# Kernel tuning notes

Hardware: AMD Instinct MI355X
Metric: run time of the kernel (lower is better)

Reference implementation:

```python
import jax, jax.numpy as jnp
import numpy as np

NUM_HEADS = 12
WIN = 7  # window_size[0] == window_size[1]


def setup_inputs() -> dict:
    key = jax.random.key(0)
    ks = jax.random.split(key, 8)
    B_, N, C = 2048, WIN * WIN, 384
    nW = 64
    return {
        "x": jax.random.normal(ks[0], (B_, N, C), dtype=jnp.float32),
        "mask": jax.random.normal(ks[1], (nW, N, N), dtype=jnp.float32),
        "qkv_w": jax.random.normal(ks[2], (3 * C, C), dtype=jnp.float32) * 0.02,
        "qkv_b": jax.random.normal(ks[3], (3 * C,), dtype=jnp.float32) * 0.02,
        "proj_w": jax.random.normal(ks[4], (C, C), dtype=jnp.float32) * 0.02,
        "proj_b": jax.random.normal(ks[5], (C,), dtype=jnp.float32) * 0.02,
        "rpb_table": jax.random.normal(ks[6], ((2 * WIN - 1) ** 2, NUM_HEADS), dtype=jnp.float32) * 0.02,
        "rel_index": jax.random.randint(ks[7], (N * N,), 0, (2 * WIN - 1) ** 2, dtype=jnp.int32),
    }


def reference(x, mask, qkv_w, qkv_b, proj_w, proj_b, rpb_table, rel_index):
    B_, N, C = x.shape
    H = NUM_HEADS
    d = C // H
    scale = d ** -0.5

    # QKV projection (quant wrappers act as identity in non-quant state)
    qkv = x @ qkv_w.T + qkv_b                      # [B_, N, 3C]
    qkv = qkv.reshape(B_, N, 3, H, d).transpose(2, 0, 3, 1, 4)  # [3, B_, H, N, d]
    q, k, v = qkv[0], qkv[1], qkv[2]

    attn = jnp.einsum("bhnd,bhmd->bhnm", q * scale, k)  # [B_, H, N, N]

    # relative position bias gather: [N*N] -> [N, N, H] -> [H, N, N]
    bias = rpb_table[rel_index].reshape(N, N, H).transpose(2, 0, 1)
    attn = attn + bias[None]

    # shifted-window mask add
    nW = mask.shape[0]
    attn = attn.reshape(B_ // nW, nW, H, N, N) + mask[None, :, None]
    attn = attn.reshape(B_, H, N, N)

    attn = jax.nn.softmax(attn, axis=-1)

    out = jnp.einsum("bhnm,bhmd->bhnd", attn, v)   # [B_, H, N, d]
    out = out.transpose(0, 2, 1, 3).reshape(B_, N, C)
    out = out @ proj_w.T + proj_b
    return out, attn
```

## Files before the change

### kernel.cpp

```cpp
#include <hip/hip_runtime.h>
#include <hip/hip_bf16.h>
#include <stdint.h>

#define H_ 12
#define D_ 32
#define N_ 49
#define C_ 384
#define B_TOT 2048
#define BH 24576
#define M_ROWS 100352
#define SCALE 0.17677669529663689f

typedef float f32x4 __attribute__((ext_vector_type(4)));
typedef __bf16 bf16x8 __attribute__((ext_vector_type(8)));
typedef unsigned short ushortx8 __attribute__((ext_vector_type(8)));

static __device__ __forceinline__ unsigned short f2bf(float f) {
  __bf16 b = (__bf16)f;
  return __builtin_bit_cast(unsigned short, b);
}

static __device__ __forceinline__ uint4 pack8(float4 a, float4 b) {
  ushortx8 v;
  v[0] = f2bf(a.x); v[1] = f2bf(a.y); v[2] = f2bf(a.z); v[3] = f2bf(a.w);
  v[4] = f2bf(b.x); v[5] = f2bf(b.y); v[6] = f2bf(b.z); v[7] = f2bf(b.w);
  return __builtin_bit_cast(uint4, v);
}

#define GL16(gp, lp)                                                        \
  __builtin_amdgcn_global_load_lds(                                         \
      (const __attribute__((address_space(1))) unsigned int*)(gp),          \
      (__attribute__((address_space(3))) unsigned int*)(lp), 16, 0, 0)

__global__ void prep(const float* __restrict__ x, const float* __restrict__ wq,
                     const float* __restrict__ wpw, const float* __restrict__ mask,
                     const float* __restrict__ rpb, const int* __restrict__ ridx,
                     unsigned short* __restrict__ x_bf,
                     unsigned short* __restrict__ wq_bf,
                     unsigned short* __restrict__ wp_bf,
                     float* __restrict__ comb) {
  const int blk = blockIdx.x, tid = threadIdx.x;
  if (blk < 2048) {
    for (int i = blk * 256 + tid; i < 4816896; i += 2048 * 256) {
      float4 a = ((const float4*)x)[2 * i];
      float4 b = ((const float4*)x)[2 * i + 1];
      *(uint4*)&x_bf[(size_t)i * 8] = pack8(a, b);
    }
  } else if (blk < 2264) {
    const int i = (blk - 2048) * 256 + tid;
    float4 a = ((const float4*)wq)[2 * i];
    float4 b = ((const float4*)wq)[2 * i + 1];
    *(uint4*)&wq_bf[(size_t)i * 8] = pack8(a, b);
  } else if (blk < 2336) {
    const int i = (blk - 2264) * 256 + tid;
    float4 a = ((const float4*)wpw)[2 * i];
    float4 b = ((const float4*)wpw)[2 * i + 1];
    *(uint4*)&wp_bf[(size_t)i * 8] = pack8(a, b);
  } else {
    const int wh = blk - 2336;
    const int w = wh / 12, h = wh - w * 12;
    float* cb = comb + (size_t)wh * 4096;
    const float* mw = mask + (size_t)w * N_ * N_;
    for (int e = tid; e < 4096; e += 256) {
      const int r = e >> 6, c = e & 63;
      float v;
      if (c >= N_) v = -1e30f;
      else if (r >= N_) v = 0.0f;
      else v = mw[r * N_ + c] + rpb[ridx[r * N_ + c] * H_ + h];
      cb[(r * 16 + (c & 15)) * 4 + (c >> 4)] = v;
    }
  }
}

__global__ __launch_bounds__(256, 4)
void qkv_gemm(const unsigned short* __restrict__ A,
              const unsigned short* __restrict__ W,
              const float* __restrict__ bias, unsigned short* __restrict__ qkv) {
  __shared__ __align__(16) unsigned short smem[16384];
  const int tid = threadIdx.x;
  const int w = blockIdx.x;
  const int t = (w & 7) * 882 + (w >> 3);
  const int bm = t / 9, bn = t - bm * 9;
  const int lane = tid & 63, wv = tid >> 6;
  const int wm = wv >> 1, wn = wv & 1;
  const int lo = lane & 15, hi = lane >> 4;

  const int sr0 = tid >> 2, sq0 = (tid & 3) ^ ((sr0 >> 1) & 3);
  const int ci1 = tid + 256;
  const int sr1 = ci1 >> 2, sq1 = (ci1 & 3) ^ ((sr1 >> 1) & 3);

  const unsigned short* Ab = A + (size_t)bm * 128 * 384;
  const unsigned short* Wb = W + (size_t)bn * 128 * 384;

  f32x4 acc[4][4];
#pragma unroll
  for (int i = 0; i < 4; i++)
#pragma unroll
    for (int j = 0; j < 4; j++)
#pragma unroll
      for (int r = 0; r < 4; r++) acc[i][j][r] = 0.0f;

  {
    unsigned short* b0 = smem;
    GL16(Ab + sr0 * 384 + sq0 * 8, b0 + tid * 8);
    GL16(Ab + sr1 * 384 + sq1 * 8, b0 + ci1 * 8);
    GL16(Wb + sr0 * 384 + sq0 * 8, b0 + 4096 + tid * 8);
    GL16(Wb + sr1 * 384 + sq1 * 8, b0 + 4096 + ci1 * 8);
  }
  __syncthreads();

  int buf = 0;
  for (int kt = 0; kt < 12; kt++) {
    if (kt < 11) {
      const int kk = (kt + 1) * 32;
      unsigned short* nb = smem + (buf ^ 1) * 8192;
      GL16(Ab + sr0 * 384 + kk + sq0 * 8, nb + tid * 8);
      GL16(Ab + sr1 * 384 + kk + sq1 * 8, nb + ci1 * 8);
      GL16(Wb + sr0 * 384 + kk + sq0 * 8, nb + 4096 + tid * 8);
      GL16(Wb + sr1 * 384 + kk + sq1 * 8, nb + 4096 + ci1 * 8);
    }
    const unsigned short* ba = smem + buf * 8192;
    bf16x8 af[4], bfm[4];
#pragma unroll
    for (int mt = 0; mt < 4; mt++) {
      const int row = wm * 64 + mt * 16 + lo;
      af[mt] = *(const bf16x8*)&ba[(row * 4 + (hi ^ ((row >> 1) & 3))) * 8];
    }
#pragma unroll
    for (int nt = 0; nt < 4; nt++) {
      const int row = wn * 64 + nt * 16 + lo;
      bfm[nt] = *(const bf16x8*)&ba[4096 + (row * 4 + (hi ^ ((row >> 1) & 3))) * 8];
    }
#pragma unroll
    for (int mt = 0; mt < 4; mt++)
#pragma unroll
      for (int nt = 0; nt < 4; nt++)
        acc[mt][nt] = __builtin_amdgcn_mfma_f32_16x16x32_bf16(af[mt], bfm[nt], acc[mt][nt], 0, 0, 0);
    __syncthreads();
    buf ^= 1;
  }

  unsigned short* ep = smem + wv * 4096;
#pragma unroll
  for (int nt = 0; nt < 4; nt++) {
    const int j = bn * 128 + wn * 64 + nt * 16 + lo;
    const float bj = bias[j];
    const float mul = (j < 384) ? SCALE : 1.0f;
    const int c16 = nt * 2 + (lo >> 3);
    const int wi = lo & 7;
#pragma unroll
    for (int mt = 0; mt < 4; mt++) {
#pragma unroll
      for (int r = 0; r < 4; r++) {
        const int row = mt * 16 + hi * 4 + r;
        ep[row * 64 + ((c16 ^ hi) << 3) + wi] = f2bf((acc[mt][nt][r] + bj) * mul);
      }
    }
  }
#pragma unroll
  for (int cc = 0; cc < 2; cc++) {
    const int cidx = cc * 64 + lane;
    const int lr = cidx >> 1, lch = cidx & 1;
    const int i = bm * 128 + wm * 64 + lr;
    const int b = i / 49, sq = i - b * 49;
    const int j0 = bn * 128 + wn * 64 + lch * 32;
    const int which = j0 / 384;
    const int rem = j0 - which * 384;
    const int h = rem >> 5;
    const int hlr = (lr >> 2) & 3;
    unsigned short* dst = qkv + ((size_t)which * BH + (size_t)b * H_ + h) * (N_ * D_) + sq * D_;
#pragma unroll
    for (int q = 0; q < 4; q++) {
      const int c16r = lch * 4 + q;
      *(uint4*)(dst + q * 8) = *(const uint4*)&ep[lr * 64 + ((c16r ^ hlr) << 3)];
    }
  }
}

__global__ __launch_bounds__(64, 2)
void attn_kernel(const unsigned short* __restrict__ qkv,
                 const float* __restrict__ comb,
                 float* __restrict__ probs,
                 unsigned short* __restrict__ av) {
  __shared__ __align__(16) unsigned short P[64 * 64];
  __shared__ __align__(16) unsigned short VT[32 * 64];
  const int lane = threadIdx.x;
  const int lo = lane & 15, hi = lane >> 4;
  const int l7 = lo & 7;
  const int h = blockIdx.x, b = blockIdx.y;

  const unsigned short* qp = qkv + (size_t)(b * H_ + h) * (N_ * D_);
  const unsigned short* kp = qp + (size_t)BH * (N_ * D_);
  const unsigned short* vp = kp + (size_t)BH * (N_ * D_);

  {
    unsigned int* vz = (unsigned int*)VT;
#pragma unroll
    for (int i = 0; i < 16; i++) vz[lane + 64 * i] = 0u;
  }
  __syncthreads();

  bf16x8 aq[4], bk[4];
#pragma unroll
  for (int t = 0; t < 4; t++) {
    aq[t] = *(const bf16x8*)(qp + (t * 16 + lo) * D_ + hi * 8);
    bk[t] = *(const bf16x8*)(kp + (t * 16 + lo) * D_ + hi * 8);
  }
  f32x4 s[4][4];
#pragma unroll
  for (int mt = 0; mt < 4; mt++)
#pragma unroll
    for (int nt = 0; nt < 4; nt++) {
#pragma unroll
      for (int r = 0; r < 4; r++) s[mt][nt][r] = 0.0f;
      s[mt][nt] = __builtin_amdgcn_mfma_f32_16x16x32_bf16(aq[mt], bk[nt], s[mt][nt], 0, 0, 0);
    }

#pragma unroll
  for (int it = 0; it < 4; it++) {
    const int idx = it * 64 + lane;
    if (idx < 196) {
      const int sq = idx >> 2, ch = idx & 3;
      ushortx8 vv = *(const ushortx8*)(vp + sq * D_ + ch * 8);
#pragma unroll
      for (int jj = 0; jj < 8; jj++)
        VT[(ch * 8 + jj) * 64 + (((sq >> 3) ^ jj) << 3) + (sq & 7)] = vv[jj];
    }
  }

  const float* cb = comb + (size_t)((b & 63) * H_ + h) * 4096;
#pragma unroll
  for (int mt = 0; mt < 4; mt++) {
#pragma unroll
    for (int r = 0; r < 4; r++) {
      const int row = mt * 16 + hi * 4 + r;
      const float4 cr = *(const float4*)(cb + (row * 16 + lo) * 4);
      float v0 = s[mt][0][r] + cr.x;
      float v1 = s[mt][1][r] + cr.y;
      float v2 = s[mt][2][r] + cr.z;
      float v3 = s[mt][3][r] + cr.w;
      float m = fmaxf(fmaxf(v0, v1), fmaxf(v2, v3));
      m = fmaxf(m, __shfl_xor(m, 1));
      m = fmaxf(m, __shfl_xor(m, 2));
      m = fmaxf(m, __shfl_xor(m, 4));
      m = fmaxf(m, __shfl_xor(m, 8));
      v0 = __expf(v0 - m); v1 = __expf(v1 - m);
      v2 = __expf(v2 - m); v3 = __expf(v3 - m);
      float sum = v0 + v1 + v2 + v3;
      sum += __shfl_xor(sum, 1);
      sum += __shfl_xor(sum, 2);
      sum += __shfl_xor(sum, 4);
      sum += __shfl_xor(sum, 8);
      const float rinv = 1.0f / sum;
      s[mt][0][r] = v0 * rinv; s[mt][1][r] = v1 * rinv;
      s[mt][2][r] = v2 * rinv; s[mt][3][r] = v3 * rinv;
    }
  }

  const size_t pbase = (size_t)(b * H_ + h) * N_ * N_;
#pragma unroll
  for (int mt = 0; mt < 4; mt++) {
#pragma unroll
    for (int r = 0; r < 4; r++) {
      const int row = mt * 16 + hi * 4 + r;
      if (row < N_) {
#pragma unroll
        for (int nt = 0; nt < 4; nt++) {
          const int c = nt * 16 + lo;
          if (c < N_) probs[pbase + row * N_ + c] = s[mt][nt][r];
        }
      }
      const int r7 = row & 7;
#pragma unroll
      for (int nt = 0; nt < 4; nt++)
        P[row * 64 + (((nt * 2 + (lo >> 3)) ^ r7) << 3) + l7] = f2bf(s[mt][nt][r]);
    }
  }
  __syncthreads();

  f32x4 o[4][2];
#pragma unroll
  for (int mt = 0; mt < 4; mt++)
#pragma unroll
    for (int n2 = 0; n2 < 2; n2++)
#pragma unroll
      for (int r = 0; r < 4; r++) o[mt][n2][r] = 0.0f;
#pragma unroll
  for (int ks = 0; ks < 2; ks++) {
    bf16x8 pa[4], vb[2];
#pragma unroll
    for (int mt = 0; mt < 4; mt++)
      pa[mt] = *(const bf16x8*)&P[(mt * 16 + lo) * 64 + (((ks * 4 + hi) ^ l7) << 3)];
#pragma unroll
    for (int n2 = 0; n2 < 2; n2++)
      vb[n2] = *(const bf16x8*)&VT[(n2 * 16 + lo) * 64 + (((ks * 4 + hi) ^ l7) << 3)];
#pragma unroll
    for (int mt = 0; mt < 4; mt++)
#pragma unroll
      for (int n2 = 0; n2 < 2; n2++)
        o[mt][n2] = __builtin_amdgcn_mfma_f32_16x16x32_bf16(pa[mt], vb[n2], o[mt][n2], 0, 0, 0);
  }

#pragma unroll
  for (int mt = 0; mt < 4; mt++) {
#pragma unroll
    for (int r = 0; r < 4; r++) {
      const int row = mt * 16 + hi * 4 + r;
      if (row < N_) {
        unsigned short* dst = av + ((size_t)b * N_ + row) * C_ + h * D_;
#pragma unroll
        for (int n2 = 0; n2 < 2; n2++)
          dst[n2 * 16 + lo] = f2bf(o[mt][n2][r]);
      }
    }
  }
}

__global__ __launch_bounds__(256, 4)
void proj_gemm(const unsigned short* __restrict__ A,
               const unsigned short* __restrict__ W,
               const float* __restrict__ bias, float* __restrict__ out) {
  __shared__ __align__(16) unsigned short smem[16384];
  const int tid = threadIdx.x;
  const int w = blockIdx.x;
  const int t = (w & 7) * 294 + (w >> 3);
  const int bm = t / 3, bn = t - bm * 3;
  const int lane = tid & 63, wv = tid >> 6;
  const int wm = wv >> 1, wn = wv & 1;
  const int lo = lane & 15, hi = lane >> 4;

  const int sr0 = tid >> 2, sq0 = (tid & 3) ^ ((sr0 >> 1) & 3);
  const int ci1 = tid + 256;
  const int sr1 = ci1 >> 2, sq1 = (ci1 & 3) ^ ((sr1 >> 1) & 3);

  const unsigned short* Ab = A + (size_t)bm * 128 * 384;
  const unsigned short* Wb = W + (size_t)bn * 128 * 384;

  f32x4 acc[4][4];
#pragma unroll
  for (int i = 0; i < 4; i++)
#pragma unroll
    for (int j = 0; j < 4; j++)
#pragma unroll
      for (int r = 0; r < 4; r++) acc[i][j][r] = 0.0f;

  {
    unsigned short* b0 = smem;
    GL16(Ab + sr0 * 384 + sq0 * 8, b0 + tid * 8);
    GL16(Ab + sr1 * 384 + sq1 * 8, b0 + ci1 * 8);
    GL16(Wb + sr0 * 384 + sq0 * 8, b0 + 4096 + tid * 8);
    GL16(Wb + sr1 * 384 + sq1 * 8, b0 + 4096 + ci1 * 8);
  }
  __syncthreads();

  int buf = 0;
  for (int kt = 0; kt < 12; kt++) {
    if (kt < 11) {
      const int kk = (kt + 1) * 32;
      unsigned short* nb = smem + (buf ^ 1) * 8192;
      GL16(Ab + sr0 * 384 + kk + sq0 * 8, nb + tid * 8);
      GL16(Ab + sr1 * 384 + kk + sq1 * 8, nb + ci1 * 8);
      GL16(Wb + sr0 * 384 + kk + sq0 * 8, nb + 4096 + tid * 8);
      GL16(Wb + sr1 * 384 + kk + sq1 * 8, nb + 4096 + ci1 * 8);
    }
    const unsigned short* ba = smem + buf * 8192;
    bf16x8 af[4], bfm[4];
#pragma unroll
    for (int mt = 0; mt < 4; mt++) {
      const int row = wm * 64 + mt * 16 + lo;
      af[mt] = *(const bf16x8*)&ba[(row * 4 + (hi ^ ((row >> 1) & 3))) * 8];
    }
#pragma unroll
    for (int nt = 0; nt < 4; nt++) {
      const int row = wn * 64 + nt * 16 + lo;
      bfm[nt] = *(const bf16x8*)&ba[4096 + (row * 4 + (hi ^ ((row >> 1) & 3))) * 8];
    }
#pragma unroll
    for (int mt = 0; mt < 4; mt++)
#pragma unroll
      for (int nt = 0; nt < 4; nt++)
        acc[mt][nt] = __builtin_amdgcn_mfma_f32_16x16x32_bf16(af[mt], bfm[nt], acc[mt][nt], 0, 0, 0);
    __syncthreads();
    buf ^= 1;
  }

#pragma unroll
  for (int nt = 0; nt < 4; nt++) {
    const int j = bn * 128 + wn * 64 + nt * 16 + lo;
    const float bj = bias[j];
#pragma unroll
    for (int mt = 0; mt < 4; mt++) {
#pragma unroll
      for (int r = 0; r < 4; r++) {
        const int i = bm * 128 + wm * 64 + mt * 16 + hi * 4 + r;
        out[(size_t)i * 384 + j] = acc[mt][nt][r] + bj;
      }
    }
  }
}

extern "C" void kernel_launch(void* const* d_in, const int* in_sizes, int n_in,
                              void* d_out, int out_size, void* d_ws, size_t ws_size,
                              hipStream_t stream) {
  const float* x      = (const float*)d_in[0];
  const float* mask   = (const float*)d_in[1];
  const float* qkv_w  = (const float*)d_in[2];
  const float* qkv_b  = (const float*)d_in[3];
  const float* proj_w = (const float*)d_in[4];
  const float* proj_b = (const float*)d_in[5];
  const float* rpb    = (const float*)d_in[6];
  const int*   ridx   = (const int*)d_in[7];

  unsigned short* qkv   = (unsigned short*)d_ws;
  unsigned short* x_bf  = qkv + (size_t)3 * BH * N_ * D_;
  unsigned short* av    = x_bf;
  float* comb           = (float*)(x_bf + (size_t)M_ROWS * C_);
  unsigned short* wq_bf = (unsigned short*)(comb + 768 * 4096);
  unsigned short* wp_bf = wq_bf + 1152 * 384;
  float* out   = (float*)d_out;
  float* probs = out + (size_t)M_ROWS * C_;

  prep<<<3104, 256, 0, stream>>>(x, qkv_w, proj_w, mask, rpb, ridx,
                                 x_bf, wq_bf, wp_bf, comb);
  qkv_gemm<<<7056, 256, 0, stream>>>(x_bf, wq_bf, qkv_b, qkv);
  attn_kernel<<<dim3(H_, B_TOT), 64, 0, stream>>>(qkv, comb, probs, av);
  proj_gemm<<<2352, 256, 0, stream>>>(av, wp_bf, proj_b, out);
}
```

Measured before the change: 461.3 us.

## Fuse window attention with output projection in one per-window kernel

```diff
diff --git a/kernel.cpp b/kernel.cpp
--- a/kernel.cpp
+++ b/kernel.cpp
@@ -177,28 +177,18 @@
   }
 }
 
-__global__ __launch_bounds__(64, 2)
-void attn_kernel(const unsigned short* __restrict__ qkv,
-                 const float* __restrict__ comb,
-                 float* __restrict__ probs,
-                 unsigned short* __restrict__ av) {
-  __shared__ __align__(16) unsigned short P[64 * 64];
-  __shared__ __align__(16) unsigned short VT[32 * 64];
-  const int lane = threadIdx.x;
+template <int HH>
+__device__ __forceinline__ void attn_head(
+    const unsigned short* __restrict__ qkv, const float* __restrict__ comb,
+    float* __restrict__ probs, unsigned short* P, unsigned short* VT,
+    int b, int wv, int lane, uint32_t* opk) {
   const int lo = lane & 15, hi = lane >> 4;
   const int l7 = lo & 7;
-  const int h = blockIdx.x, b = blockIdx.y;
+  const int h = wv * 2 + HH;
 
   const unsigned short* qp = qkv + (size_t)(b * H_ + h) * (N_ * D_);
   const unsigned short* kp = qp + (size_t)BH * (N_ * D_);
   const unsigned short* vp = kp + (size_t)BH * (N_ * D_);
-
-  {
-    unsigned int* vz = (unsigned int*)VT;
-#pragma unroll
-    for (int i = 0; i < 16; i++) vz[lane + 64 * i] = 0u;
-  }
-  __syncthreads();
 
   bf16x8 aq[4], bk[4];
 #pragma unroll
@@ -276,7 +266,6 @@
         P[row * 64 + (((nt * 2 + (lo >> 3)) ^ r7) << 3) + l7] = f2bf(s[mt][nt][r]);
     }
   }
-  __syncthreads();
 
   f32x4 o[4][2];
 #pragma unroll
@@ -302,40 +291,66 @@
   }
 
 #pragma unroll
-  for (int mt = 0; mt < 4; mt++) {
-#pragma unroll
-    for (int r = 0; r < 4; r++) {
-      const int row = mt * 16 + hi * 4 + r;
-      if (row < N_) {
-        unsigned short* dst = av + ((size_t)b * N_ + row) * C_ + h * D_;
-#pragma unroll
-        for (int n2 = 0; n2 < 2; n2++)
-          dst[n2 * 16 + lo] = f2bf(o[mt][n2][r]);
+  for (int mt = 0; mt < 4; mt++)
+#pragma unroll
+    for (int n2 = 0; n2 < 2; n2++)
+#pragma unroll
+      for (int p = 0; p < 2; p++)
+        opk[mt * 4 + n2 * 2 + p] =
+            (uint32_t)f2bf(o[mt][n2][2 * p]) |
+            ((uint32_t)f2bf(o[mt][n2][2 * p + 1]) << 16);
+}
+
+__global__ __launch_bounds__(384, 3)
+void attn_proj(const unsigned short* __restrict__ qkv,
+               const float* __restrict__ comb,
+               const unsigned short* __restrict__ wp,
+               const float* __restrict__ pbias,
+               float* __restrict__ probs,
+               float* __restrict__ out) {
+  __shared__ __align__(16) unsigned short smem[36864];
+  const int tid = threadIdx.x;
+  const int wv = tid / 64, lane = tid & 63;
+  const int lo = lane & 15, hi = lane >> 4;
+  const int b = blockIdx.x;
+  unsigned short* P = smem + wv * 4096;
+  unsigned short* VT = smem + 24576 + wv * 2048;
+  unsigned short* avl = smem;
+
+  {
+    unsigned int* vz = (unsigned int*)VT;
+#pragma unroll
+    for (int i = 0; i < 16; i++) vz[lane + 64 * i] = 0u;
+  }
+
+  uint32_t opk_all[32];
+  attn_head<0>(qkv, comb, probs, P, VT, b, wv, lane, &opk_all[0]);
+  attn_head<1>(qkv, comb, probs, P, VT, b, wv, lane, &opk_all[16]);
+
+  __syncthreads();
+
+#pragma unroll
+  for (int hh = 0; hh < 2; hh++) {
+    const int col0 = (wv * 2 + hh) * 32;
+#pragma unroll
+    for (int mt = 0; mt < 4; mt++)
+#pragma unroll
+      for (int n2 = 0; n2 < 2; n2++) {
+        const int col = col0 + n2 * 16 + lo;
+        const int c16 = col >> 3, c7 = col & 7;
+#pragma unroll
+        for (int p = 0; p < 2; p++) {
+          const uint32_t v = opk_all[hh * 16 + mt * 4 + n2 * 2 + p];
+          const int row0 = mt * 16 + hi * 4 + 2 * p;
+          avl[row0 * 384 + ((c16 ^ (row0 & 7)) << 3) + c7] = (unsigned short)v;
+          const int row1 = row0 + 1;
+          avl[row1 * 384 + ((c16 ^ (row1 & 7)) << 3) + c7] = (unsigned short)(v >> 16);
+        }
       }
-    }
-  }
-}
-
-__global__ __launch_bounds__(256, 4)
-void proj_gemm(const unsigned short* __restrict__ A,
-               const unsigned short* __restrict__ W,
-               const float* __restrict__ bias, float* __restrict__ out) {
-  __shared__ __align__(16) unsigned short smem[16384];
-  const int tid = threadIdx.x;
-  const int w = blockIdx.x;
-  const int t = (w & 7) * 294 + (w >> 3);
-  const int bm = t / 3, bn = t - bm * 3;
-  const int lane = tid & 63, wv = tid >> 6;
-  const int wm = wv >> 1, wn = wv & 1;
-  const int lo = lane & 15, hi = lane >> 4;
-
-  const int sr0 = tid >> 2, sq0 = (tid & 3) ^ ((sr0 >> 1) & 3);
-  const int ci1 = tid + 256;
-  const int sr1 = ci1 >> 2, sq1 = (ci1 & 3) ^ ((sr1 >> 1) & 3);
-
-  const unsigned short* Ab = A + (size_t)bm * 128 * 384;
-  const unsigned short* Wb = W + (size_t)bn * 128 * 384;
-
+  }
+  __syncthreads();
+
+  const int jb = wv * 64;
   f32x4 acc[4][4];
 #pragma unroll
   for (int i = 0; i < 4; i++)
@@ -344,56 +359,35 @@
 #pragma unroll
       for (int r = 0; r < 4; r++) acc[i][j][r] = 0.0f;
 
-  {
-    unsigned short* b0 = smem;
-    GL16(Ab + sr0 * 384 + sq0 * 8, b0 + tid * 8);
-    GL16(Ab + sr1 * 384 + sq1 * 8, b0 + ci1 * 8);
-    GL16(Wb + sr0 * 384 + sq0 * 8, b0 + 4096 + tid * 8);
-    GL16(Wb + sr1 * 384 + sq1 * 8, b0 + 4096 + ci1 * 8);
-  }
-  __syncthreads();
-
-  int buf = 0;
   for (int kt = 0; kt < 12; kt++) {
-    if (kt < 11) {
-      const int kk = (kt + 1) * 32;
-      unsigned short* nb = smem + (buf ^ 1) * 8192;
-      GL16(Ab + sr0 * 384 + kk + sq0 * 8, nb + tid * 8);
-      GL16(Ab + sr1 * 384 + kk + sq1 * 8, nb + ci1 * 8);
-      GL16(Wb + sr0 * 384 + kk + sq0 * 8, nb + 4096 + tid * 8);
-      GL16(Wb + sr1 * 384 + kk + sq1 * 8, nb + 4096 + ci1 * 8);
-    }
-    const unsigned short* ba = smem + buf * 8192;
-    bf16x8 af[4], bfm[4];
+    bf16x8 af[4], bf[4];
 #pragma unroll
     for (int mt = 0; mt < 4; mt++) {
-      const int row = wm * 64 + mt * 16 + lo;
-      af[mt] = *(const bf16x8*)&ba[(row * 4 + (hi ^ ((row >> 1) & 3))) * 8];
-    }
-#pragma unroll
-    for (int nt = 0; nt < 4; nt++) {
-      const int row = wn * 64 + nt * 16 + lo;
-      bfm[nt] = *(const bf16x8*)&ba[4096 + (row * 4 + (hi ^ ((row >> 1) & 3))) * 8];
-    }
+      const int row = mt * 16 + lo;
+      const int chn = ((kt * 4 + hi) ^ (row & 7));
+      af[mt] = *(const bf16x8*)&avl[row * 384 + chn * 8];
+    }
+#pragma unroll
+    for (int nt = 0; nt < 4; nt++)
+      bf[nt] = *(const bf16x8*)(wp + (size_t)(jb + nt * 16 + lo) * 384 + kt * 32 + hi * 8);
 #pragma unroll
     for (int mt = 0; mt < 4; mt++)
 #pragma unroll
       for (int nt = 0; nt < 4; nt++)
-        acc[mt][nt] = __builtin_amdgcn_mfma_f32_16x16x32_bf16(af[mt], bfm[nt], acc[mt][nt], 0, 0, 0);
-    __syncthreads();
-    buf ^= 1;
+        acc[mt][nt] = __builtin_amdgcn_mfma_f32_16x16x32_bf16(af[mt], bf[nt], acc[mt][nt], 0, 0, 0);
   }
 
 #pragma unroll
   for (int nt = 0; nt < 4; nt++) {
-    const int j = bn * 128 + wn * 64 + nt * 16 + lo;
-    const float bj = bias[j];
+    const int j = jb + nt * 16 + lo;
+    const float bj = pbias[j];
 #pragma unroll
     for (int mt = 0; mt < 4; mt++) {
 #pragma unroll
       for (int r = 0; r < 4; r++) {
-        const int i = bm * 128 + wm * 64 + mt * 16 + hi * 4 + r;
-        out[(size_t)i * 384 + j] = acc[mt][nt][r] + bj;
+        const int row = mt * 16 + hi * 4 + r;
+        if (row < N_)
+          out[((size_t)b * N_ + row) * C_ + j] = acc[mt][nt][r] + bj;
       }
     }
   }
@@ -413,7 +407,6 @@
 
   unsigned short* qkv   = (unsigned short*)d_ws;
   unsigned short* x_bf  = qkv + (size_t)3 * BH * N_ * D_;
-  unsigned short* av    = x_bf;
   float* comb           = (float*)(x_bf + (size_t)M_ROWS * C_);
   unsigned short* wq_bf = (unsigned short*)(comb + 768 * 4096);
   unsigned short* wp_bf = wq_bf + 1152 * 384;
@@ -423,6 +416,5 @@
   prep<<<3104, 256, 0, stream>>>(x, qkv_w, proj_w, mask, rpb, ridx,
                                  x_bf, wq_bf, wp_bf, comb);
   qkv_gemm<<<7056, 256, 0, stream>>>(x_bf, wq_bf, qkv_b, qkv);
-  attn_kernel<<<dim3(H_, B_TOT), 64, 0, stream>>>(qkv, comb, probs, av);
-  proj_gemm<<<2352, 256, 0, stream>>>(av, wp_bf, proj_b, out);
-}
+  attn_proj<<<2048, 384, 0, stream>>>(qkv, comb, wp_bf, proj_b, probs, out);
+}
```

Result: slower. 743.5 us (+61.2%).
